# Kernel optimization log

Hardware: AMD Instinct MI355X
Metric: run time of the kernel (lower is better)

## Reference

```python
import jax, jax.numpy as jnp
import numpy as np

NS, NT, DF, H, O = 200000, 50000, 20, 64, 64
NE, NL = 1000000, 500000


def setup_inputs() -> dict:
    key = jax.random.key(0)
    ks = jax.random.split(key, 24)
    inp = {
        'target_x': jax.random.normal(ks[0], (NT, DF), jnp.float32),
        'source_node_id': jnp.arange(NS, dtype=jnp.int64),
        'target_node_id': jnp.arange(NT, dtype=jnp.int64),
        'edge_src': jax.random.randint(ks[1], (NE,), 0, NS),
        'edge_dst': jax.random.randint(ks[2], (NE,), 0, NT),
        'label_src': jax.random.randint(ks[3], (NL,), 0, NS),
        'label_dst': jax.random.randint(ks[4], (NL,), 0, NT),
        'src_emb': jax.random.normal(ks[5], (NS, H), jnp.float32) * 0.05,
        'tgt_emb': jax.random.normal(ks[6], (NT, H), jnp.float32) * 0.05,
        'lin_W': jax.random.normal(ks[7], (DF, H), jnp.float32) * 0.05,
        'lin_b': jnp.zeros((H,), jnp.float32),
    }
    # SAGEConv params: (Wl, bl, Wr) per edge type per layer. st = source->target, ts = target->source
    dims = {'st1': (H, H), 'ts1': (H, H), 'st2': (H, O), 'ts2': (H, O)}
    i = 8
    for name, (din, dout) in dims.items():
        inp['Wl_' + name] = jax.random.normal(ks[i], (din, dout), jnp.float32) * 0.05
        inp['bl_' + name] = jnp.zeros((dout,), jnp.float32)
        inp['Wr_' + name] = jax.random.normal(ks[i + 1], (din, dout), jnp.float32) * 0.05
        i += 2
    return inp


def _sage(x_src, x_dst, src_idx, dst_idx, n_dst, Wl, bl, Wr):
    # PyG SAGEConv, aggr='mean': lin_l(mean_{j in N(i)} x_j) + lin_r(x_i)
    msg = x_src[src_idx]                                   # [E, d] gather
    agg = jax.ops.segment_sum(msg, dst_idx, num_segments=n_dst)
    deg = jax.ops.segment_sum(jnp.ones((src_idx.shape[0],), x_src.dtype), dst_idx, num_segments=n_dst)
    mean = agg / jnp.maximum(deg, 1.0)[:, None]
    return mean @ Wl + bl + x_dst @ Wr


def reference(target_x, source_node_id, target_node_id, edge_src, edge_dst,
              label_src, label_dst, src_emb, tgt_emb, lin_W, lin_b,
              Wl_st1, bl_st1, Wr_st1, Wl_ts1, bl_ts1, Wr_ts1,
              Wl_st2, bl_st2, Wr_st2, Wl_ts2, bl_ts2, Wr_ts2):
    ns, nt = src_emb.shape[0], tgt_emb.shape[0]
    x_s = src_emb[source_node_id]                          # [NS, H]
    x_t = target_x @ lin_W + lin_b + tgt_emb[target_node_id]  # [NT, H]
    # layer 1 (per edge type, summed per dst type; each dst type has one incoming type)
    h_t = _sage(x_s, x_t, edge_src, edge_dst, nt, Wl_st1, bl_st1, Wr_st1)
    h_s = _sage(x_t, x_s, edge_dst, edge_src, ns, Wl_ts1, bl_ts1, Wr_ts1)
    h_t, h_s = jax.nn.relu(h_t), jax.nn.relu(h_s)
    # layer 2
    o_t = _sage(h_s, h_t, edge_src, edge_dst, nt, Wl_st2, bl_st2, Wr_st2)
    o_s = _sage(h_t, h_s, edge_dst, edge_src, ns, Wl_ts2, bl_ts2, Wr_ts2)
    # dot-product link classifier
    return (o_s[label_src] * o_t[label_dst]).sum(axis=-1)  # [NL]
```

## Files before the change

kernel.cpp:

```cpp
#include <hip/hip_runtime.h>

#define NSRC 200000
#define NTGT 50000
#define DF   20
#define HD   64
#define NE   1000000
#define NL   500000

#define SH_T 6
#define SH_S 8
#define NB   782
#define CHUNK 8192
#define NCH  ((NE + CHUNK - 1) / CHUNK)

typedef unsigned short ushort_t;
typedef short s16x8 __attribute__((ext_vector_type(8)));
typedef float f32x4 __attribute__((ext_vector_type(4)));

__device__ __forceinline__ float bf2f(ushort_t u) {
    return __uint_as_float(((unsigned)u) << 16);
}
__device__ __forceinline__ ushort_t f2bf(float f) {
    unsigned u = __float_as_uint(f);
    return (ushort_t)((u + 0x7fffu + ((u >> 16) & 1u)) >> 16);
}

__global__ __launch_bounds__(1024) void chunk_hist(
    const int* __restrict__ es, const int* __restrict__ ed, int ne,
    int* __restrict__ cnt_t, int* __restrict__ cnt_s)
{
    __shared__ int h[NB];
    const int dir  = blockIdx.y;
    const int c    = blockIdx.x;
    const int base = c * CHUNK;
    const int n    = min(CHUNK, ne - base);
    const int* key = dir ? es : ed;
    const int sh   = dir ? SH_S : SH_T;
    int* cnt       = dir ? cnt_s : cnt_t;

    for (int i = threadIdx.x; i < NB; i += 1024) h[i] = 0;
    __syncthreads();
    for (int i = threadIdx.x; i < n; i += 1024)
        atomicAdd(&h[key[base + i] >> sh], 1);
    __syncthreads();
    for (int i = threadIdx.x; i < NB; i += 1024) cnt[c * NB + i] = h[i];
}

__global__ __launch_bounds__(1024) void chunk_scan(
    int* __restrict__ cnt_t, int* __restrict__ cnt_s,
    int* __restrict__ bt_t, int* __restrict__ bt_s)
{
    int* cnt = blockIdx.x ? cnt_s : cnt_t;
    int* bt  = blockIdx.x ? bt_s  : bt_t;
    const int b = threadIdx.x;
    if (b < NB) {
        int run = 0;
        for (int c = 0; c < NCH; ++c) {
            int v = cnt[c * NB + b];
            cnt[c * NB + b] = run;
            run += v;
        }
        bt[b] = run;
    }
}

__global__ __launch_bounds__(1024) void bucket_scan(
    const int* __restrict__ bt_t, int* __restrict__ bb_t,
    const int* __restrict__ bt_s, int* __restrict__ bb_s)
{
    const int* bt = blockIdx.x ? bt_s : bt_t;
    int* bb       = blockIdx.x ? bb_s : bb_t;

    __shared__ int s[1024];
    const int tid = threadIdx.x;
    int v = (tid < NB) ? bt[tid] : 0;
    s[tid] = v;
    __syncthreads();
    for (int d = 1; d < 1024; d <<= 1) {
        int t = (tid >= d) ? s[tid - d] : 0;
        __syncthreads();
        s[tid] += t;
        __syncthreads();
    }
    int incl = s[tid];
    if (tid < NB) bb[tid] = incl - v;
    if (tid == NB - 1) bb[NB] = incl;
}

__global__ __launch_bounds__(1024) void bin_fill2(
    const int* __restrict__ es, const int* __restrict__ ed, int ne,
    const int* __restrict__ cnt_t, const int* __restrict__ cnt_s,
    const int* __restrict__ bb_t, const int* __restrict__ bb_s,
    int2* __restrict__ pairs_t, int2* __restrict__ pairs_s)
{
    __shared__ int cur[NB];
    const int dir  = blockIdx.y;
    const int c    = blockIdx.x;
    const int base = c * CHUNK;
    const int n    = min(CHUNK, ne - base);
    const int* key = dir ? es : ed;
    const int* oth = dir ? ed : es;
    const int sh   = dir ? SH_S : SH_T;
    const int* cnt = dir ? cnt_s : cnt_t;
    const int* bb  = dir ? bb_s  : bb_t;
    int2* pairs    = dir ? pairs_s : pairs_t;

    for (int i = threadIdx.x; i < NB; i += 1024)
        cur[i] = bb[i] + cnt[c * NB + i];
    __syncthreads();
    for (int i = threadIdx.x; i < n; i += 1024) {
        int k = key[base + i], o = oth[base + i];
        int p = atomicAdd(&cur[k >> sh], 1);
        pairs[p] = make_int2(o, k);
    }
}

template <int SHIFT>
__global__ __launch_bounds__(256) void bucket_build(
    const int2* __restrict__ pairs, const int* __restrict__ bb,
    int* __restrict__ rp, int* __restrict__ col, int n, int ne)
{
    __shared__ int hist[256];
    __shared__ int scn[256];
    __shared__ int cur[256];
    const int b = blockIdx.x;
    const int tid = threadIdx.x;
    const int beg = bb[b], end = bb[b + 1];
    const int row0 = b << SHIFT;

    hist[tid] = 0;
    __syncthreads();
    for (int e = beg + tid; e < end; e += 256)
        atomicAdd(&hist[pairs[e].y - row0], 1);
    __syncthreads();

    int v = hist[tid];
    scn[tid] = v;
    __syncthreads();
    for (int d = 1; d < 256; d <<= 1) {
        int t = (tid >= d) ? scn[tid - d] : 0;
        __syncthreads();
        scn[tid] += t;
        __syncthreads();
    }
    int ex = scn[tid] - v;
    cur[tid] = ex;
    int row = row0 + tid;
    if (tid < (1 << SHIFT) && row < n) rp[row] = beg + ex;
    if (b == 0 && tid == 0) rp[n] = ne;
    __syncthreads();

    for (int e = beg + tid; e < end; e += 256) {
        int2 pr = pairs[e];
        int p = atomicAdd(&cur[pr.y - row0], 1);
        col[beg + p] = pr.x;
    }
}

__global__ void prep_features(const float* __restrict__ tx, const float* __restrict__ W,
                              const float* __restrict__ b, const float* __restrict__ temb,
                              const float* __restrict__ semb,
                              ushort_t* __restrict__ xb, ushort_t* __restrict__ sb)
{
    int stride = gridDim.x * blockDim.x;
    int id = blockIdx.x * blockDim.x + threadIdx.x;
    for (int i = id; i < NTGT * HD; i += stride) {
        int n = i >> 6, k = i & 63;
        float acc = b[k] + temb[i];
#pragma unroll
        for (int d = 0; d < DF; ++d) acc += tx[n * DF + d] * W[d * HD + k];
        xb[i] = f2bf(acc);
    }
    for (int i = id; i < NSRC * HD; i += stride) sb[i] = f2bf(semb[i]);
}

__global__ void pack_weights(
    const float* __restrict__ Wl0, const float* __restrict__ Wr0,
    const float* __restrict__ Wl1, const float* __restrict__ Wr1,
    const float* __restrict__ Wl2, const float* __restrict__ Wr2,
    const float* __restrict__ Wl3, const float* __restrict__ Wr3,
    ushort_t* __restrict__ wt)
{
    int i = blockIdx.x * blockDim.x + threadIdx.x;
    if (i >= 4 * 64 * 128) return;
    int set = i >> 13, rem = i & 8191;
    int j = rem >> 7, k = rem & 127;
    const float* Wl = set == 0 ? Wl0 : set == 1 ? Wl1 : set == 2 ? Wl2 : Wl3;
    const float* Wr = set == 0 ? Wr0 : set == 1 ? Wr1 : set == 2 ? Wr2 : Wr3;
    float v = (k < 64) ? Wl[k * 64 + j] : Wr[(k - 64) * 64 + j];
    wt[i] = f2bf(v);
}

template <bool RELU>
__global__ __launch_bounds__(256) void sage_tile(
    const ushort_t* __restrict__ table, const int* __restrict__ rp,
    const int* __restrict__ col, const ushort_t* __restrict__ xd,
    const ushort_t* __restrict__ wt, const float* __restrict__ bl,
    ushort_t* __restrict__ out, int n)
{
    __shared__ ushort_t smean[64][72];
    const int tid  = threadIdx.x;
    const int el   = tid & 7;
    const int ew   = tid >> 3;
    const int d0   = el * 8;
    const int base = blockIdx.x * 64;

#pragma unroll
    for (int half = 0; half < 2; ++half) {
        const int row  = ew + half * 32;
        const int node = base + row;
        s16x8 o = {0, 0, 0, 0, 0, 0, 0, 0};
        if (node < n) {
            const int beg = rp[node], end = rp[node + 1];
            float a0[8], a1[8], a2[8], a3[8];
#pragma unroll
            for (int i = 0; i < 8; ++i) { a0[i] = 0.f; a1[i] = 0.f; a2[i] = 0.f; a3[i] = 0.f; }
            int e = beg;
            for (; e + 4 <= end; e += 4) {
                int c0 = col[e], c1 = col[e + 1], c2 = col[e + 2], c3 = col[e + 3];
                s16x8 v0 = *(const s16x8*)&table[(size_t)c0 * HD + d0];
                s16x8 v1 = *(const s16x8*)&table[(size_t)c1 * HD + d0];
                s16x8 v2 = *(const s16x8*)&table[(size_t)c2 * HD + d0];
                s16x8 v3 = *(const s16x8*)&table[(size_t)c3 * HD + d0];
#pragma unroll
                for (int i = 0; i < 8; ++i) {
                    a0[i] += bf2f((ushort_t)v0[i]);
                    a1[i] += bf2f((ushort_t)v1[i]);
                    a2[i] += bf2f((ushort_t)v2[i]);
                    a3[i] += bf2f((ushort_t)v3[i]);
                }
            }
            for (; e < end; ++e) {
                s16x8 v = *(const s16x8*)&table[(size_t)col[e] * HD + d0];
#pragma unroll
                for (int i = 0; i < 8; ++i) a0[i] += bf2f((ushort_t)v[i]);
            }
            float degf = (float)(end - beg);
            float inv  = degf > 0.f ? 1.f / degf : 0.f;
#pragma unroll
            for (int i = 0; i < 8; ++i)
                o[i] = (short)f2bf((a0[i] + a1[i] + a2[i] + a3[i]) * inv);
        }
        *(s16x8*)&smean[row][d0] = o;
    }
    __syncthreads();

    const int lane = tid & 63;
    const int wid  = tid >> 6;
    const int lr   = lane & 15;
    const int kg   = lane >> 4;

    s16x8 b[4][4];
#pragma unroll
    for (int jb = 0; jb < 4; ++jb)
#pragma unroll
        for (int kb = 0; kb < 4; ++kb)
            b[jb][kb] = *(const s16x8*)&wt[(jb * 16 + lr) * 128 + kb * 32 + kg * 8];

    float bias[4];
#pragma unroll
    for (int jb = 0; jb < 4; ++jb) bias[jb] = bl[jb * 16 + lr];

    const int arow = base + wid * 16 + lr;
    s16x8 a[4];
    a[0] = *(const s16x8*)&smean[wid * 16 + lr][kg * 8];
    a[1] = *(const s16x8*)&smean[wid * 16 + lr][32 + kg * 8];
    if (arow < n) {
        const ushort_t* xrow = xd + (size_t)arow * HD;
        a[2] = *(const s16x8*)(xrow + kg * 8);
        a[3] = *(const s16x8*)(xrow + 32 + kg * 8);
    } else {
        s16x8 z = {0, 0, 0, 0, 0, 0, 0, 0};
        a[2] = z; a[3] = z;
    }

    const int drow0 = base + wid * 16 + kg * 4;
#pragma unroll
    for (int jb = 0; jb < 4; ++jb) {
        f32x4 acc = {bias[jb], bias[jb], bias[jb], bias[jb]};
#pragma unroll
        for (int kb = 0; kb < 4; ++kb)
            acc = __builtin_amdgcn_mfma_f32_16x16x32_bf16(a[kb], b[jb][kb], acc, 0, 0, 0);
#pragma unroll
        for (int r = 0; r < 4; ++r) {
            int nn = drow0 + r;
            if (nn < n) {
                float v = acc[r];
                if (RELU) v = fmaxf(v, 0.f);
                out[(size_t)nn * HD + jb * 16 + lr] = f2bf(v);
            }
        }
    }
}

__global__ __launch_bounds__(256) void classify_b(
    const ushort_t* __restrict__ os, const ushort_t* __restrict__ ot,
    const int* __restrict__ ls, const int* __restrict__ lt,
    float* __restrict__ out, int nl)
{
    const int lane = threadIdx.x & 63;
    const int sub  = lane >> 4;
    const int g    = (lane & 15) * 4;
    int w = (blockIdx.x * blockDim.x + threadIdx.x) >> 6;
    const int wstride = (gridDim.x * blockDim.x) >> 6;

    for (int l0 = w * 8; l0 < nl; l0 += wstride * 8) {
        int la = l0 + sub;
        int lb = l0 + 4 + sub;
        float pa = 0.f, pb = 0.f;
        if (la < nl) {
            int a = ls[la], b = lt[la];
            ushort4 va = *(const ushort4*)&os[(size_t)a * HD + g];
            ushort4 vb = *(const ushort4*)&ot[(size_t)b * HD + g];
            pa = bf2f(va.x) * bf2f(vb.x) + bf2f(va.y) * bf2f(vb.y)
               + bf2f(va.z) * bf2f(vb.z) + bf2f(va.w) * bf2f(vb.w);
        }
        if (lb < nl) {
            int a = ls[lb], b = lt[lb];
            ushort4 va = *(const ushort4*)&os[(size_t)a * HD + g];
            ushort4 vb = *(const ushort4*)&ot[(size_t)b * HD + g];
            pb = bf2f(va.x) * bf2f(vb.x) + bf2f(va.y) * bf2f(vb.y)
               + bf2f(va.z) * bf2f(vb.z) + bf2f(va.w) * bf2f(vb.w);
        }
#pragma unroll
        for (int o = 8; o > 0; o >>= 1) {
            pa += __shfl_xor(pa, o, 64);
            pb += __shfl_xor(pb, o, 64);
        }
        if ((lane & 15) == 0) {
            if (la < nl) out[la] = pa;
            if (lb < nl) out[lb] = pb;
        }
    }
}

extern "C" void kernel_launch(void* const* d_in, const int* in_sizes, int n_in,
                              void* d_out, int out_size, void* d_ws, size_t ws_size,
                              hipStream_t stream)
{
    const float* target_x = (const float*)d_in[0];
    const int* edge_src  = (const int*)d_in[3];
    const int* edge_dst  = (const int*)d_in[4];
    const int* label_src = (const int*)d_in[5];
    const int* label_dst = (const int*)d_in[6];
    const float* src_emb = (const float*)d_in[7];
    const float* tgt_emb = (const float*)d_in[8];
    const float* lin_W   = (const float*)d_in[9];
    const float* lin_b   = (const float*)d_in[10];
    const float* Wl_st1 = (const float*)d_in[11];
    const float* bl_st1 = (const float*)d_in[12];
    const float* Wr_st1 = (const float*)d_in[13];
    const float* Wl_ts1 = (const float*)d_in[14];
    const float* bl_ts1 = (const float*)d_in[15];
    const float* Wr_ts1 = (const float*)d_in[16];
    const float* Wl_st2 = (const float*)d_in[17];
    const float* bl_st2 = (const float*)d_in[18];
    const float* Wr_st2 = (const float*)d_in[19];
    const float* Wl_ts2 = (const float*)d_in[20];
    const float* bl_ts2 = (const float*)d_in[21];
    const float* Wr_ts2 = (const float*)d_in[22];
    float* out = (float*)d_out;

    char* ws = (char*)d_ws;
    size_t off = 0;
    auto take = [&](size_t bytes) -> char* {
        char* p = ws + off;
        off = (off + bytes + 255) & ~(size_t)255;
        return p;
    };
    int* cnt_t = (int*)take((size_t)NCH * NB * 4);
    int* cnt_s = (int*)take((size_t)NCH * NB * 4);
    int* bt_t  = (int*)take((size_t)NB * 4);
    int* bt_s  = (int*)take((size_t)NB * 4);
    int* bb_t  = (int*)take((size_t)(NB + 1) * 4);
    int* bb_s  = (int*)take((size_t)(NB + 1) * 4);
    int* rp_t  = (int*)take((size_t)(NTGT + 1) * 4);
    int* rp_s  = (int*)take((size_t)(NSRC + 1) * 4);
    int* col_t = (int*)take((size_t)NE * 4);
    int* col_s = (int*)take((size_t)NE * 4);
    int2* pairs_t = (int2*)take((size_t)NE * 8);
    int2* pairs_s = (int2*)take((size_t)NE * 8);
    ushort_t* wt   = (ushort_t*)take((size_t)4 * 64 * 128 * 2);
    ushort_t* xb_t = (ushort_t*)take((size_t)NTGT * HD * 2);
    ushort_t* sb   = (ushort_t*)take((size_t)NSRC * HD * 2);
    ushort_t* hb_t = (ushort_t*)take((size_t)NTGT * HD * 2);
    ushort_t* hb_s = (ushort_t*)take((size_t)NSRC * HD * 2);
    ushort_t* ob_t = (ushort_t*)take((size_t)NTGT * HD * 2);
    ushort_t* ob_s = (ushort_t*)take((size_t)NSRC * HD * 2);

    dim3 gch(NCH, 2);
    chunk_hist<<<gch, 1024, 0, stream>>>(edge_src, edge_dst, NE, cnt_t, cnt_s);
    chunk_scan<<<2, 1024, 0, stream>>>(cnt_t, cnt_s, bt_t, bt_s);
    bucket_scan<<<2, 1024, 0, stream>>>(bt_t, bb_t, bt_s, bb_s);
    bin_fill2<<<gch, 1024, 0, stream>>>(edge_src, edge_dst, NE,
                                        cnt_t, cnt_s, bb_t, bb_s, pairs_t, pairs_s);
    bucket_build<SH_T><<<NB, 256, 0, stream>>>(pairs_t, bb_t, rp_t, col_t, NTGT, NE);
    bucket_build<SH_S><<<NB, 256, 0, stream>>>(pairs_s, bb_s, rp_s, col_s, NSRC, NE);

    pack_weights<<<128, 256, 0, stream>>>(Wl_st1, Wr_st1, Wl_ts1, Wr_ts1,
                                          Wl_st2, Wr_st2, Wl_ts2, Wr_ts2, wt);
    prep_features<<<2048, 256, 0, stream>>>(target_x, lin_W, lin_b, tgt_emb,
                                            src_emb, xb_t, sb);

    const int GT = (NTGT + 63) / 64;
    const int GS = (NSRC + 63) / 64;

    sage_tile<true><<<GT, 256, 0, stream>>>(sb,   rp_t, col_t, xb_t,
                                            wt + 0 * 8192, bl_st1, hb_t, NTGT);
    sage_tile<true><<<GS, 256, 0, stream>>>(xb_t, rp_s, col_s, sb,
                                            wt + 1 * 8192, bl_ts1, hb_s, NSRC);
    sage_tile<false><<<GT, 256, 0, stream>>>(hb_s, rp_t, col_t, hb_t,
                                             wt + 2 * 8192, bl_st2, ob_t, NTGT);
    sage_tile<false><<<GS, 256, 0, stream>>>(hb_t, rp_s, col_s, hb_s,
                                             wt + 3 * 8192, bl_ts2, ob_s, NSRC);

    classify_b<<<2048, 256, 0, stream>>>(ob_s, ob_t, label_src, label_dst, out, NL);
}
```

Measured before the change: 295.8 us.

## Merge independent kernels and interleave target/source SAGE tiles per layer

Fuses the histogram, feature prep and weight packing into one launch, merges the two scan kernels, and merges the two bucket_build launches. Each SAGE layer's target and source passes now run as one launch, with blocks interleaved 1:4 between the target and source graphs. The gather loop is also restructured to process two rows' edges concurrently with clamped indices, to raise memory-level parallelism. The aim is fewer launches and gaps, at the cost of more branching and register pressure in the gather loop.

```diff
diff --git a/kernel.cpp b/kernel.cpp
--- a/kernel.cpp
+++ b/kernel.cpp
@@ -13,6 +13,12 @@
 #define CHUNK 8192
 #define NCH  ((NE + CHUNK - 1) / CHUNK)
 
+#define HIST_BLKS (NCH * 2)
+#define PREP_BLKS 256
+
+#define GT 782
+#define GS 3125
+
 typedef unsigned short ushort_t;
 typedef short s16x8 __attribute__((ext_vector_type(8)));
 typedef float f32x4 __attribute__((ext_vector_type(4)));
@@ -25,56 +31,78 @@
     return (ushort_t)((u + 0x7fffu + ((u >> 16) & 1u)) >> 16);
 }
 
-__global__ __launch_bounds__(1024) void chunk_hist(
-    const int* __restrict__ es, const int* __restrict__ ed, int ne,
-    int* __restrict__ cnt_t, int* __restrict__ cnt_s)
+__global__ __launch_bounds__(1024) void front(
+    const int* __restrict__ es, const int* __restrict__ ed,
+    int* __restrict__ cnt_t, int* __restrict__ cnt_s,
+    const float* __restrict__ tx, const float* __restrict__ W,
+    const float* __restrict__ lb, const float* __restrict__ temb,
+    const float* __restrict__ semb,
+    ushort_t* __restrict__ xb, ushort_t* __restrict__ sbuf,
+    const float* __restrict__ Wl0, const float* __restrict__ Wr0,
+    const float* __restrict__ Wl1, const float* __restrict__ Wr1,
+    const float* __restrict__ Wl2, const float* __restrict__ Wr2,
+    const float* __restrict__ Wl3, const float* __restrict__ Wr3,
+    ushort_t* __restrict__ wt)
 {
     __shared__ int h[NB];
-    const int dir  = blockIdx.y;
-    const int c    = blockIdx.x;
-    const int base = c * CHUNK;
-    const int n    = min(CHUNK, ne - base);
-    const int* key = dir ? es : ed;
-    const int sh   = dir ? SH_S : SH_T;
-    int* cnt       = dir ? cnt_s : cnt_t;
-
-    for (int i = threadIdx.x; i < NB; i += 1024) h[i] = 0;
-    __syncthreads();
-    for (int i = threadIdx.x; i < n; i += 1024)
-        atomicAdd(&h[key[base + i] >> sh], 1);
-    __syncthreads();
-    for (int i = threadIdx.x; i < NB; i += 1024) cnt[c * NB + i] = h[i];
-}
-
-__global__ __launch_bounds__(1024) void chunk_scan(
+    const int b   = blockIdx.x;
+    const int tid = threadIdx.x;
+
+    if (b < HIST_BLKS) {
+        const int dir  = b / NCH;
+        const int c    = b % NCH;
+        const int base = c * CHUNK;
+        const int n    = min(CHUNK, NE - base);
+        const int* key = dir ? es : ed;
+        const int sh   = dir ? SH_S : SH_T;
+        int* cnt       = dir ? cnt_s : cnt_t;
+
+        for (int i = tid; i < NB; i += 1024) h[i] = 0;
+        __syncthreads();
+        for (int i = tid; i < n; i += 1024)
+            atomicAdd(&h[key[base + i] >> sh], 1);
+        __syncthreads();
+        for (int i = tid; i < NB; i += 1024) cnt[c * NB + i] = h[i];
+    } else if (b < HIST_BLKS + PREP_BLKS) {
+        const int id   = (b - HIST_BLKS) * 1024 + tid;
+        const int pstr = PREP_BLKS * 1024;
+        for (int i = id; i < NTGT * HD; i += pstr) {
+            int n = i >> 6, k = i & 63;
+            float acc = lb[k] + temb[i];
+#pragma unroll
+            for (int d = 0; d < DF; ++d) acc += tx[n * DF + d] * W[d * HD + k];
+            xb[i] = f2bf(acc);
+        }
+        for (int i = id; i < NSRC * HD; i += pstr) sbuf[i] = f2bf(semb[i]);
+    } else {
+        for (int i = tid; i < 4 * 64 * 128; i += 1024) {
+            int set = i >> 13, rem = i & 8191;
+            int j = rem >> 7, k = rem & 127;
+            const float* Wl = set == 0 ? Wl0 : set == 1 ? Wl1 : set == 2 ? Wl2 : Wl3;
+            const float* Wr = set == 0 ? Wr0 : set == 1 ? Wr1 : set == 2 ? Wr2 : Wr3;
+            float v = (k < 64) ? Wl[k * 64 + j] : Wr[(k - 64) * 64 + j];
+            wt[i] = f2bf(v);
+        }
+    }
+}
+
+__global__ __launch_bounds__(1024) void scan_all(
     int* __restrict__ cnt_t, int* __restrict__ cnt_s,
-    int* __restrict__ bt_t, int* __restrict__ bt_s)
+    int* __restrict__ bb_t, int* __restrict__ bb_s)
 {
     int* cnt = blockIdx.x ? cnt_s : cnt_t;
-    int* bt  = blockIdx.x ? bt_s  : bt_t;
-    const int b = threadIdx.x;
-    if (b < NB) {
-        int run = 0;
-        for (int c = 0; c < NCH; ++c) {
-            int v = cnt[c * NB + b];
-            cnt[c * NB + b] = run;
-            run += v;
-        }
-        bt[b] = run;
-    }
-}
-
-__global__ __launch_bounds__(1024) void bucket_scan(
-    const int* __restrict__ bt_t, int* __restrict__ bb_t,
-    const int* __restrict__ bt_s, int* __restrict__ bb_s)
-{
-    const int* bt = blockIdx.x ? bt_s : bt_t;
-    int* bb       = blockIdx.x ? bb_s : bb_t;
-
+    int* bb  = blockIdx.x ? bb_s  : bb_t;
     __shared__ int s[1024];
     const int tid = threadIdx.x;
-    int v = (tid < NB) ? bt[tid] : 0;
-    s[tid] = v;
+    int run = 0;
+    if (tid < NB) {
+        for (int c = 0; c < NCH; ++c) {
+            int v = cnt[c * NB + tid];
+            cnt[c * NB + tid] = run;
+            run += v;
+        }
+    }
+    s[tid] = (tid < NB) ? run : 0;
     __syncthreads();
     for (int d = 1; d < 1024; d <<= 1) {
         int t = (tid >= d) ? s[tid - d] : 0;
@@ -83,12 +111,12 @@
         __syncthreads();
     }
     int incl = s[tid];
-    if (tid < NB) bb[tid] = incl - v;
+    if (tid < NB) bb[tid] = incl - run;
     if (tid == NB - 1) bb[NB] = incl;
 }
 
 __global__ __launch_bounds__(1024) void bin_fill2(
-    const int* __restrict__ es, const int* __restrict__ ed, int ne,
+    const int* __restrict__ es, const int* __restrict__ ed,
     const int* __restrict__ cnt_t, const int* __restrict__ cnt_s,
     const int* __restrict__ bb_t, const int* __restrict__ bb_s,
     int2* __restrict__ pairs_t, int2* __restrict__ pairs_s)
@@ -97,7 +125,7 @@
     const int dir  = blockIdx.y;
     const int c    = blockIdx.x;
     const int base = c * CHUNK;
-    const int n    = min(CHUNK, ne - base);
+    const int n    = min(CHUNK, NE - base);
     const int* key = dir ? es : ed;
     const int* oth = dir ? ed : es;
     const int sh   = dir ? SH_S : SH_T;
@@ -115,18 +143,27 @@
     }
 }
 
-template <int SHIFT>
-__global__ __launch_bounds__(256) void bucket_build(
-    const int2* __restrict__ pairs, const int* __restrict__ bb,
-    int* __restrict__ rp, int* __restrict__ col, int n, int ne)
+__global__ __launch_bounds__(256) void bucket_build_all(
+    const int2* __restrict__ pairs_t, const int* __restrict__ bb_t,
+    int* __restrict__ rp_t, int* __restrict__ col_t,
+    const int2* __restrict__ pairs_s, const int* __restrict__ bb_s,
+    int* __restrict__ rp_s, int* __restrict__ col_s)
 {
     __shared__ int hist[256];
     __shared__ int scn[256];
     __shared__ int cur[256];
-    const int b = blockIdx.x;
+    const bool is_t = blockIdx.x < NB;
+    const int b = is_t ? blockIdx.x : blockIdx.x - NB;
+    const int2* pairs = is_t ? pairs_t : pairs_s;
+    const int* bb     = is_t ? bb_t : bb_s;
+    int* rp           = is_t ? rp_t : rp_s;
+    int* col          = is_t ? col_t : col_s;
+    const int shift   = is_t ? SH_T : SH_S;
+    const int n       = is_t ? NTGT : NSRC;
+
     const int tid = threadIdx.x;
     const int beg = bb[b], end = bb[b + 1];
-    const int row0 = b << SHIFT;
+    const int row0 = b << shift;
 
     hist[tid] = 0;
     __syncthreads();
@@ -146,8 +183,8 @@
     int ex = scn[tid] - v;
     cur[tid] = ex;
     int row = row0 + tid;
-    if (tid < (1 << SHIFT) && row < n) rp[row] = beg + ex;
-    if (b == 0 && tid == 0) rp[n] = ne;
+    if (tid < (1 << shift) && row < n) rp[row] = beg + ex;
+    if (b == 0 && tid == 0) rp[n] = NE;
     __syncthreads();
 
     for (int e = beg + tid; e < end; e += 256) {
@@ -157,92 +194,96 @@
     }
 }
 
-__global__ void prep_features(const float* __restrict__ tx, const float* __restrict__ W,
-                              const float* __restrict__ b, const float* __restrict__ temb,
-                              const float* __restrict__ semb,
-                              ushort_t* __restrict__ xb, ushort_t* __restrict__ sb)
-{
-    int stride = gridDim.x * blockDim.x;
-    int id = blockIdx.x * blockDim.x + threadIdx.x;
-    for (int i = id; i < NTGT * HD; i += stride) {
-        int n = i >> 6, k = i & 63;
-        float acc = b[k] + temb[i];
-#pragma unroll
-        for (int d = 0; d < DF; ++d) acc += tx[n * DF + d] * W[d * HD + k];
-        xb[i] = f2bf(acc);
-    }
-    for (int i = id; i < NSRC * HD; i += stride) sb[i] = f2bf(semb[i]);
-}
-
-__global__ void pack_weights(
-    const float* __restrict__ Wl0, const float* __restrict__ Wr0,
-    const float* __restrict__ Wl1, const float* __restrict__ Wr1,
-    const float* __restrict__ Wl2, const float* __restrict__ Wr2,
-    const float* __restrict__ Wl3, const float* __restrict__ Wr3,
-    ushort_t* __restrict__ wt)
-{
-    int i = blockIdx.x * blockDim.x + threadIdx.x;
-    if (i >= 4 * 64 * 128) return;
-    int set = i >> 13, rem = i & 8191;
-    int j = rem >> 7, k = rem & 127;
-    const float* Wl = set == 0 ? Wl0 : set == 1 ? Wl1 : set == 2 ? Wl2 : Wl3;
-    const float* Wr = set == 0 ? Wr0 : set == 1 ? Wr1 : set == 2 ? Wr2 : Wr3;
-    float v = (k < 64) ? Wl[k * 64 + j] : Wr[(k - 64) * 64 + j];
-    wt[i] = f2bf(v);
-}
-
 template <bool RELU>
-__global__ __launch_bounds__(256) void sage_tile(
-    const ushort_t* __restrict__ table, const int* __restrict__ rp,
-    const int* __restrict__ col, const ushort_t* __restrict__ xd,
-    const ushort_t* __restrict__ wt, const float* __restrict__ bl,
-    ushort_t* __restrict__ out, int n)
+__global__ __launch_bounds__(256) void sage_layer(
+    const ushort_t* __restrict__ tab_t, const int* __restrict__ rp_t,
+    const int* __restrict__ col_t, const ushort_t* __restrict__ xd_t,
+    const ushort_t* __restrict__ wt_t, const float* __restrict__ bl_t,
+    ushort_t* __restrict__ out_t,
+    const ushort_t* __restrict__ tab_s, const int* __restrict__ rp_s,
+    const int* __restrict__ col_s, const ushort_t* __restrict__ xd_s,
+    const ushort_t* __restrict__ wt_s, const float* __restrict__ bl_s,
+    ushort_t* __restrict__ out_s)
 {
     __shared__ ushort_t smean[64][72];
-    const int tid  = threadIdx.x;
-    const int el   = tid & 7;
-    const int ew   = tid >> 3;
-    const int d0   = el * 8;
-    const int base = blockIdx.x * 64;
-
-#pragma unroll
-    for (int half = 0; half < 2; ++half) {
-        const int row  = ew + half * 32;
-        const int node = base + row;
-        s16x8 o = {0, 0, 0, 0, 0, 0, 0, 0};
-        if (node < n) {
-            const int beg = rp[node], end = rp[node + 1];
-            float a0[8], a1[8], a2[8], a3[8];
-#pragma unroll
-            for (int i = 0; i < 8; ++i) { a0[i] = 0.f; a1[i] = 0.f; a2[i] = 0.f; a3[i] = 0.f; }
-            int e = beg;
-            for (; e + 4 <= end; e += 4) {
-                int c0 = col[e], c1 = col[e + 1], c2 = col[e + 2], c3 = col[e + 3];
-                s16x8 v0 = *(const s16x8*)&table[(size_t)c0 * HD + d0];
-                s16x8 v1 = *(const s16x8*)&table[(size_t)c1 * HD + d0];
-                s16x8 v2 = *(const s16x8*)&table[(size_t)c2 * HD + d0];
-                s16x8 v3 = *(const s16x8*)&table[(size_t)c3 * HD + d0];
-#pragma unroll
-                for (int i = 0; i < 8; ++i) {
-                    a0[i] += bf2f((ushort_t)v0[i]);
-                    a1[i] += bf2f((ushort_t)v1[i]);
-                    a2[i] += bf2f((ushort_t)v2[i]);
-                    a3[i] += bf2f((ushort_t)v3[i]);
-                }
-            }
-            for (; e < end; ++e) {
-                s16x8 v = *(const s16x8*)&table[(size_t)col[e] * HD + d0];
-#pragma unroll
-                for (int i = 0; i < 8; ++i) a0[i] += bf2f((ushort_t)v[i]);
-            }
-            float degf = (float)(end - beg);
-            float inv  = degf > 0.f ? 1.f / degf : 0.f;
-#pragma unroll
-            for (int i = 0; i < 8; ++i)
-                o[i] = (short)f2bf((a0[i] + a1[i] + a2[i] + a3[i]) * inv);
-        }
-        *(s16x8*)&smean[row][d0] = o;
-    }
+    const int blk = blockIdx.x;
+    const bool is_t = (blk % 5 == 0);
+    const int bi = is_t ? blk / 5 : blk - blk / 5 - 1;
+
+    const ushort_t* table = is_t ? tab_t : tab_s;
+    const int* rp         = is_t ? rp_t  : rp_s;
+    const int* col        = is_t ? col_t : col_s;
+    const ushort_t* xd    = is_t ? xd_t  : xd_s;
+    const ushort_t* wt    = is_t ? wt_t  : wt_s;
+    const float* bl       = is_t ? bl_t  : bl_s;
+    ushort_t* out         = is_t ? out_t : out_s;
+    const int n           = is_t ? NTGT  : NSRC;
+
+    const int tid = threadIdx.x;
+    const int el  = tid & 7;
+    const int ew  = tid >> 3;
+    const int d0  = el * 8;
+    const int base = bi * 64;
+
+    const int node0 = base + ew;
+    const int node1 = base + ew + 32;
+    int e0 = 0, end0 = 0, e1 = 0, end1 = 0;
+    if (node0 < n) { e0 = rp[node0]; end0 = rp[node0 + 1]; }
+    if (node1 < n) { e1 = rp[node1]; end1 = rp[node1 + 1]; }
+    const float inv0 = (end0 > e0) ? 1.f / (float)(end0 - e0) : 0.f;
+    const float inv1 = (end1 > e1) ? 1.f / (float)(end1 - e1) : 0.f;
+
+    float r0[4][8], r1[4][8];
+#pragma unroll
+    for (int s = 0; s < 4; ++s)
+#pragma unroll
+        for (int i = 0; i < 8; ++i) { r0[s][i] = 0.f; r1[s][i] = 0.f; }
+
+    while (e0 < end0 || e1 < end1) {
+        const bool w0 = e0 < end0, w1 = e1 < end1;
+        s16x8 v0[4], v1[4];
+        if (w0) {
+            int c[4];
+#pragma unroll
+            for (int s = 0; s < 4; ++s) c[s] = col[min(e0 + s, end0 - 1)];
+#pragma unroll
+            for (int s = 0; s < 4; ++s)
+                v0[s] = *(const s16x8*)&table[(size_t)c[s] * HD + d0];
+        }
+        if (w1) {
+            int c[4];
+#pragma unroll
+            for (int s = 0; s < 4; ++s) c[s] = col[min(e1 + s, end1 - 1)];
+#pragma unroll
+            for (int s = 0; s < 4; ++s)
+                v1[s] = *(const s16x8*)&table[(size_t)c[s] * HD + d0];
+        }
+        if (w0) {
+#pragma unroll
+            for (int s = 0; s < 4; ++s)
+                if (e0 + s < end0)
+#pragma unroll
+                    for (int i = 0; i < 8; ++i) r0[s][i] += bf2f((ushort_t)v0[s][i]);
+            e0 += 4;
+        }
+        if (w1) {
+#pragma unroll
+            for (int s = 0; s < 4; ++s)
+                if (e1 + s < end1)
+#pragma unroll
+                    for (int i = 0; i < 8; ++i) r1[s][i] += bf2f((ushort_t)v1[s][i]);
+            e1 += 4;
+        }
+    }
+
+    s16x8 o0, o1;
+#pragma unroll
+    for (int i = 0; i < 8; ++i) {
+        o0[i] = (short)f2bf((r0[0][i] + r0[1][i] + r0[2][i] + r0[3][i]) * inv0);
+        o1[i] = (short)f2bf((r1[0][i] + r1[1][i] + r1[2][i] + r1[3][i]) * inv1);
+    }
+    *(s16x8*)&smean[ew][d0] = o0;
+    *(s16x8*)&smean[ew + 32][d0] = o1;
     __syncthreads();
 
     const int lane = tid & 63;
@@ -250,12 +291,12 @@
     const int lr   = lane & 15;
     const int kg   = lane >> 4;
 
-    s16x8 b[4][4];
+    s16x8 bfr[4][4];
 #pragma unroll
     for (int jb = 0; jb < 4; ++jb)
 #pragma unroll
         for (int kb = 0; kb < 4; ++kb)
-            b[jb][kb] = *(const s16x8*)&wt[(jb * 16 + lr) * 128 + kb * 32 + kg * 8];
+            bfr[jb][kb] = *(const s16x8*)&wt[(jb * 16 + lr) * 128 + kb * 32 + kg * 8];
 
     float bias[4];
 #pragma unroll
@@ -280,7 +321,7 @@
         f32x4 acc = {bias[jb], bias[jb], bias[jb], bias[jb]};
 #pragma unroll
         for (int kb = 0; kb < 4; ++kb)
-            acc = __builtin_amdgcn_mfma_f32_16x16x32_bf16(a[kb], b[jb][kb], acc, 0, 0, 0);
+            acc = __builtin_amdgcn_mfma_f32_16x16x32_bf16(a[kb], bfr[jb][kb], acc, 0, 0, 0);
 #pragma unroll
         for (int r = 0; r < 4; ++r) {
             int nn = drow0 + r;
@@ -370,8 +411,6 @@
     };
     int* cnt_t = (int*)take((size_t)NCH * NB * 4);
     int* cnt_s = (int*)take((size_t)NCH * NB * 4);
-    int* bt_t  = (int*)take((size_t)NB * 4);
-    int* bt_s  = (int*)take((size_t)NB * 4);
     int* bb_t  = (int*)take((size_t)(NB + 1) * 4);
     int* bb_s  = (int*)take((size_t)(NB + 1) * 4);
     int* rp_t  = (int*)take((size_t)(NTGT + 1) * 4);
@@ -388,31 +427,24 @@
     ushort_t* ob_t = (ushort_t*)take((size_t)NTGT * HD * 2);
     ushort_t* ob_s = (ushort_t*)take((size_t)NSRC * HD * 2);
 
+    front<<<HIST_BLKS + PREP_BLKS + 1, 1024, 0, stream>>>(
+        edge_src, edge_dst, cnt_t, cnt_s,
+        target_x, lin_W, lin_b, tgt_emb, src_emb, xb_t, sb,
+        Wl_st1, Wr_st1, Wl_ts1, Wr_ts1, Wl_st2, Wr_st2, Wl_ts2, Wr_ts2, wt);
+
+    scan_all<<<2, 1024, 0, stream>>>(cnt_t, cnt_s, bb_t, bb_s);
     dim3 gch(NCH, 2);
-    chunk_hist<<<gch, 1024, 0, stream>>>(edge_src, edge_dst, NE, cnt_t, cnt_s);
-    chunk_scan<<<2, 1024, 0, stream>>>(cnt_t, cnt_s, bt_t, bt_s);
-    bucket_scan<<<2, 1024, 0, stream>>>(bt_t, bb_t, bt_s, bb_s);
-    bin_fill2<<<gch, 1024, 0, stream>>>(edge_src, edge_dst, NE,
+    bin_fill2<<<gch, 1024, 0, stream>>>(edge_src, edge_dst,
                                         cnt_t, cnt_s, bb_t, bb_s, pairs_t, pairs_s);
-    bucket_build<SH_T><<<NB, 256, 0, stream>>>(pairs_t, bb_t, rp_t, col_t, NTGT, NE);
-    bucket_build<SH_S><<<NB, 256, 0, stream>>>(pairs_s, bb_s, rp_s, col_s, NSRC, NE);
-
-    pack_weights<<<128, 256, 0, stream>>>(Wl_st1, Wr_st1, Wl_ts1, Wr_ts1,
-                                          Wl_st2, Wr_st2, Wl_ts2, Wr_ts2, wt);
-    prep_features<<<2048, 256, 0, stream>>>(target_x, lin_W, lin_b, tgt_emb,
-                                            src_emb, xb_t, sb);
-
-    const int GT = (NTGT + 63) / 64;
-    const int GS = (NSRC + 63) / 64;
-
-    sage_tile<true><<<GT, 256, 0, stream>>>(sb,   rp_t, col_t, xb_t,
-                                            wt + 0 * 8192, bl_st1, hb_t, NTGT);
-    sage_tile<true><<<GS, 256, 0, stream>>>(xb_t, rp_s, col_s, sb,
-                                            wt + 1 * 8192, bl_ts1, hb_s, NSRC);
-    sage_tile<false><<<GT, 256, 0, stream>>>(hb_s, rp_t, col_t, hb_t,
-                                             wt + 2 * 8192, bl_st2, ob_t, NTGT);
-    sage_tile<false><<<GS, 256, 0, stream>>>(hb_t, rp_s, col_s, hb_s,
-                                             wt + 3 * 8192, bl_ts2, ob_s, NSRC);
+    bucket_build_all<<<2 * NB, 256, 0, stream>>>(pairs_t, bb_t, rp_t, col_t,
+                                                 pairs_s, bb_s, rp_s, col_s);
+
+    sage_layer<true><<<GT + GS, 256, 0, stream>>>(
+        sb,   rp_t, col_t, xb_t, wt + 0 * 8192, bl_st1, hb_t,
+        xb_t, rp_s, col_s, sb,   wt + 1 * 8192, bl_ts1, hb_s);
+    sage_layer<false><<<GT + GS, 256, 0, stream>>>(
+        hb_s, rp_t, col_t, hb_t, wt + 2 * 8192, bl_st2, ob_t,
+        hb_t, rp_s, col_s, hb_s, wt + 3 * 8192, bl_ts2, ob_s);
 
     classify_b<<<2048, 256, 0, stream>>>(ob_s, ob_t, label_src, label_dst, out, NL);
 }
```

After: 277.8 us. -6.1%, faster.
